# Kernel optimization log

Hardware: AMD Instinct MI355X
Metric: run time of the kernel (lower is better)

Reference implementation:

```python
import jax, jax.numpy as jnp
import numpy as np

N = 50000      # nodes
E = 800000     # edges (avg degree 16)
IN = 128       # in_dim = num_heads * out_dim
H = 8          # num_heads
D = 16         # out_dim per head
R = 9          # num_rels = num_bases


def setup_inputs() -> dict:
    key = jax.random.key(0)
    ks = jax.random.split(key, 13)
    sw = 1.0 / np.sqrt(IN)
    sc = 1.0 / np.sqrt(R)
    return {
        "h": jax.random.normal(ks[0], (N, IN), jnp.float32),
        "Qw": jax.random.normal(ks[1], (R, IN, IN), jnp.float32) * sw,
        "Qc": jax.random.normal(ks[2], (R, R), jnp.float32) * sc,
        "Qb": jax.random.normal(ks[3], (IN,), jnp.float32) * 0.02,
        "Kw": jax.random.normal(ks[4], (R, IN, IN), jnp.float32) * sw,
        "Kc": jax.random.normal(ks[5], (R, R), jnp.float32) * sc,
        "Kb": jax.random.normal(ks[6], (IN,), jnp.float32) * 0.02,
        "Vw": jax.random.normal(ks[7], (R, IN, IN), jnp.float32) * sw,
        "Vc": jax.random.normal(ks[8], (R, R), jnp.float32) * sc,
        "Vb": jax.random.normal(ks[9], (IN,), jnp.float32) * 0.02,
        "src": jax.random.randint(ks[10], (E,), 0, N, jnp.int32),
        "dst": jax.random.randint(ks[11], (E,), 0, N, jnp.int32),
        "etype": jax.random.randint(ks[12], (E,), 0, R, jnp.int32),
    }


def _rel_graph_conv(x, w_basis, comb, bias, src, dst, etype):
    # basis decomposition: W_r = sum_b comb[r,b] * basis[b]  -> [R, IN, IN]
    W = jnp.einsum("rb,bio->rio", comb, w_basis)
    # project node features under every relation once: [R, N, IN]
    xW = jnp.einsum("ni,rio->rno", x, W)
    # per-edge message m_e = W_{etype_e} x_{src_e}
    msg = xW[etype, src]                                   # [E, IN]
    agg = jax.ops.segment_sum(msg, dst, num_segments=N)    # sum over incoming edges
    return jax.nn.relu(agg + bias)                         # dropout = eval mode (identity)


def reference(h, Qw, Qc, Qb, Kw, Kc, Kb, Vw, Vc, Vb, src, dst, etype):
    Q = _rel_graph_conv(h, Qw, Qc, Qb, src, dst, etype).reshape(N, H, D)
    K = _rel_graph_conv(h, Kw, Kc, Kb, src, dst, etype).reshape(N, H, D)
    V = _rel_graph_conv(h, Vw, Vc, Vb, src, dst, etype).reshape(N, H, D)
    # edge attention score: (K_src . Q_dst) per head, scaled + clamped exp
    score = jnp.sum(K[src] * Q[dst], axis=-1, keepdims=True) / np.sqrt(D)  # [E, H, 1]
    score = jnp.exp(jnp.clip(score, -10.0, 10.0))
    # weighted-V aggregation and normalizer via segment sums over dst
    wV = jax.ops.segment_sum(V[src] * score, dst, num_segments=N)  # [N, H, D]
    z = jax.ops.segment_sum(score, dst, num_segments=N)            # [N, H, 1]
    return wV / (z + 1e-6)
```

## Files before the change

kernel.cpp:

```cpp
#include <hip/hip_runtime.h>

#define NN 50000
#define NE 800000
#define IND 128
#define NH 8
#define DH 16
#define NR 9
#define KTOT 1152
#define NOUT 384
#define OB_N 24
#define NBLK 196

typedef __attribute__((ext_vector_type(8))) short bf16x8;
typedef __attribute__((ext_vector_type(4))) float f32x4;

__device__ __forceinline__ ushort f2bf(float x) {
  unsigned u = __float_as_uint(x);
  u += 0x7FFF + ((u >> 16) & 1);
  return (ushort)(u >> 16);
}
__device__ __forceinline__ float bf2f(ushort h) {
  return __uint_as_float(((unsigned)h) << 16);
}

__global__ __launch_bounds__(256) void make_w(const float* __restrict__ Qw, const float* __restrict__ Qc,
                                              const float* __restrict__ Kw, const float* __restrict__ Kc,
                                              const float* __restrict__ Vw, const float* __restrict__ Vc,
                                              ushort* __restrict__ Wh, ushort* __restrict__ Wl) {
  int t = blockIdx.x * 256 + threadIdx.x;
  int k = t / NOUT;
  int og = t % NOUT;
  int r = k >> 7, i = k & 127;
  int m = og >> 7, oc = og & 127;
  const float* basis = m == 0 ? Qw : m == 1 ? Kw : Vw;
  const float* comb  = m == 0 ? Qc : m == 1 ? Kc : Vc;
  float w = 0.f;
#pragma unroll
  for (int b = 0; b < NR; ++b)
    w += comb[r * NR + b] * basis[(long)b * IND * IND + i * IND + oc];
  ushort hi = f2bf(w);
  ushort lo = f2bf(w - bf2f(hi));
  long idx = ((long)(k >> 5) * OB_N + (og >> 4)) * 512
           + (((k >> 3) & 3) * 16 + (og & 15)) * 8 + (k & 7);
  Wh[idx] = hi;
  Wl[idx] = lo;
}

__global__ __launch_bounds__(256) void hist_dst(const int* __restrict__ dst,
                                                int* __restrict__ deg) {
  int e = blockIdx.x * 256 + threadIdx.x;
  if (e < NE) atomicAdd(&deg[dst[e]], 1);
}

__global__ __launch_bounds__(256) void scan_p1(const int* __restrict__ deg,
                                               int* __restrict__ bsum) {
  __shared__ int sb[256];
  int t = threadIdx.x;
  int idx = blockIdx.x * 256 + t;
  int v = (idx < NN) ? deg[idx] : 0;
  sb[t] = v;
  __syncthreads();
  for (int off = 128; off > 0; off >>= 1) {
    if (t < off) sb[t] += sb[t + off];
    __syncthreads();
  }
  if (t == 0) bsum[blockIdx.x] = sb[0];
}

__global__ __launch_bounds__(256) void scan_p2(const int* __restrict__ bsum,
                                               int* __restrict__ boff,
                                               int* __restrict__ rowptr) {
  __shared__ int sb[256];
  int t = threadIdx.x;
  int v = (t < NBLK) ? bsum[t] : 0;
  sb[t] = v;
  __syncthreads();
  for (int off = 1; off < 256; off <<= 1) {
    int add = (t >= off) ? sb[t - off] : 0;
    __syncthreads();
    sb[t] += add;
    __syncthreads();
  }
  if (t < NBLK) boff[t] = sb[t] - v;
  if (t == 0) rowptr[NN] = NE;
}

__global__ __launch_bounds__(256) void scan_p3(const int* __restrict__ deg,
                                               const int* __restrict__ boff,
                                               int* __restrict__ rowptr,
                                               int* __restrict__ cursor) {
  __shared__ int sb[256];
  int t = threadIdx.x;
  int idx = blockIdx.x * 256 + t;
  int v = (idx < NN) ? deg[idx] : 0;
  sb[t] = v;
  __syncthreads();
  for (int off = 1; off < 256; off <<= 1) {
    int add = (t >= off) ? sb[t - off] : 0;
    __syncthreads();
    sb[t] += add;
    __syncthreads();
  }
  if (idx < NN) {
    int excl = sb[t] - v + boff[blockIdx.x];
    rowptr[idx] = excl;
    cursor[idx] = excl;
  }
}

__global__ __launch_bounds__(256) void bucket_edges(const int* __restrict__ src,
                                                    const int* __restrict__ dst,
                                                    const int* __restrict__ et,
                                                    int* __restrict__ cursor,
                                                    int* __restrict__ epk) {
  int e = blockIdx.x * 256 + threadIdx.x;
  if (e >= NE) return;
  int d = dst[e];
  int pos = atomicAdd(&cursor[d], 1);
  epk[pos] = src[e] | (et[e] << 20);
}

__global__ __launch_bounds__(256) void conv_agg(const float* __restrict__ x,
                                                const int* __restrict__ rowptr,
                                                const int* __restrict__ epk,
                                                ushort* __restrict__ Ah,
                                                ushort* __restrict__ Al,
                                                int rlo, int rhi) {
  int wid = (blockIdx.x * 256 + threadIdx.x) >> 6;
  int lane = threadIdx.x & 63;
  if (wid >= NN) return;
  float ax[NR], ay[NR];
#pragma unroll
  for (int rr = 0; rr < NR; ++rr) { ax[rr] = 0.f; ay[rr] = 0.f; }
  int r0 = rowptr[wid], r1 = rowptr[wid + 1];
  for (int base = r0; base < r1; base += 64) {
    int pe = (base + lane < r1) ? epk[base + lane] : 0;
    int cnt = min(64, r1 - base);
    for (int j = 0; j < cnt; ++j) {
      int p = __shfl(pe, j);
      int s = p & 0xFFFFF;
      int r = p >> 20;
      float2 xv = *(const float2*)(x + (long)s * IND + lane * 2);
#pragma unroll
      for (int rr = 0; rr < NR; ++rr)
        if (r == rr) { ax[rr] += xv.x; ay[rr] += xv.y; }
    }
  }
#pragma unroll
  for (int rr = 0; rr < NR; ++rr)
    if (rr >= rlo && rr < rhi) {
      ushort h0 = f2bf(ax[rr]);
      ushort l0 = f2bf(ax[rr] - bf2f(h0));
      ushort h1 = f2bf(ay[rr]);
      ushort l1 = f2bf(ay[rr] - bf2f(h1));
      long o = ((long)(rr - rlo) * NN + wid) * IND + lane * 2;
      *(unsigned*)(Ah + o) = (unsigned)h0 | ((unsigned)h1 << 16);
      *(unsigned*)(Al + o) = (unsigned)l0 | ((unsigned)l1 << 16);
    }
}

__global__ __launch_bounds__(512) void gemm_mfma(const ushort* __restrict__ Ah,
                                                 const ushort* __restrict__ Al,
                                                 const ushort* __restrict__ Wh,
                                                 const ushort* __restrict__ Wl,
                                                 const float* __restrict__ Qb,
                                                 const float* __restrict__ Kb,
                                                 const float* __restrict__ Vb,
                                                 float* __restrict__ F,
                                                 int nrel, int rlo, int first, int last) {
  const int tid = threadIdx.x;
  const int lane = tid & 63;
  const int wid = tid >> 6;
  const int wr = wid >> 2;
  const int wc = wid & 3;
  const int n0 = blockIdx.x * 128 + wr * 64;
  const int l15 = lane & 15;
  const int kg = lane >> 4;
  const int kgofs = kg * 8;

  long rowOff[4];
#pragma unroll
  for (int mi = 0; mi < 4; ++mi)
    rowOff[mi] = (long)min(n0 + mi * 16 + l15, NN - 1) * IND;

  const int nsteps = nrel * 4;

  f32x4 acc[4][6];
#pragma unroll
  for (int mi = 0; mi < 4; ++mi)
#pragma unroll
    for (int ni = 0; ni < 6; ++ni) acc[mi][ni] = (f32x4){0.f, 0.f, 0.f, 0.f};

  bf16x8 a0[8], a1[8], w[12];

  auto LOADA = [&](bf16x8* A, int s) {
    const long ab = ((long)(s >> 2) * NN) * IND + ((s & 3) * 32 + kgofs);
#pragma unroll
    for (int mi = 0; mi < 4; ++mi) {
      A[mi]     = *(const bf16x8*)(Ah + ab + rowOff[mi]);
      A[4 + mi] = *(const bf16x8*)(Al + ab + rowOff[mi]);
    }
  };
  auto LOADW = [&](bf16x8* W, int s) {
    const long wb = (((long)(rlo * 4 + s) * OB_N + wc * 6) * 64 + lane) * 8;
#pragma unroll
    for (int ni = 0; ni < 6; ++ni) {
      W[ni]     = *(const bf16x8*)(Wh + wb + ni * 512);
      W[6 + ni] = *(const bf16x8*)(Wl + wb + ni * 512);
    }
  };
  auto DOMFMA = [&](bf16x8* A, bf16x8* W) {
#pragma unroll
    for (int ni = 0; ni < 6; ++ni)
#pragma unroll
      for (int mi = 0; mi < 4; ++mi) {
        acc[mi][ni] = __builtin_amdgcn_mfma_f32_16x16x32_bf16(A[mi],     W[6 + ni], acc[mi][ni], 0, 0, 0);
        acc[mi][ni] = __builtin_amdgcn_mfma_f32_16x16x32_bf16(A[4 + mi], W[ni],     acc[mi][ni], 0, 0, 0);
        acc[mi][ni] = __builtin_amdgcn_mfma_f32_16x16x32_bf16(A[mi],     W[ni],     acc[mi][ni], 0, 0, 0);
      }
  };

  LOADA(a0, 0);
  LOADW(w, 0);
  for (int s = 0; s < nsteps; s += 2) {
    LOADA(a1, s + 1);
    DOMFMA(a0, w);
    LOADW(w, s + 1);
    if (s + 2 < nsteps) LOADA(a0, s + 2);
    DOMFMA(a1, w);
    if (s + 2 < nsteps) LOADW(w, s + 2);
  }

#pragma unroll
  for (int mi = 0; mi < 4; ++mi) {
#pragma unroll
    for (int ni = 0; ni < 6; ++ni) {
      int og = wc * 96 + ni * 16 + l15;
      int m = og >> 7, oc = og & 127;
      float b = (m == 0 ? Qb : m == 1 ? Kb : Vb)[oc];
      float* Fm = F + (long)m * NN * IND;
#pragma unroll
      for (int reg = 0; reg < 4; ++reg) {
        int n = n0 + mi * 16 + kg * 4 + reg;
        if (n < NN) {
          long fo = (long)n * IND + oc;
          float v = acc[mi][ni][reg];
          if (!first) v += Fm[fo];
          if (last) { v += b; v = v > 0.f ? v : 0.f; }
          Fm[fo] = v;
        }
      }
    }
  }
}

__global__ __launch_bounds__(256) void node_attn(const float* __restrict__ Q,
                                                 const float* __restrict__ K,
                                                 const float* __restrict__ V,
                                                 const int* __restrict__ rowptr,
                                                 const int* __restrict__ epk,
                                                 float* __restrict__ out) {
  int wid = (blockIdx.x * 256 + threadIdx.x) >> 6;
  int lane = threadIdx.x & 63;
  if (wid >= NN) return;
  float2 q = *(const float2*)(Q + (long)wid * IND + lane * 2);
  float accx = 0.f, accy = 0.f, zacc = 0.f;
  int r0 = rowptr[wid], r1 = rowptr[wid + 1];
  for (int base = r0; base < r1; base += 64) {
    int pe = (base + lane < r1) ? epk[base + lane] : 0;
    int cnt = min(64, r1 - base);
    for (int j = 0; j < cnt; ++j) {
      int s = __shfl(pe, j) & 0xFFFFF;
      float2 k = *(const float2*)(K + (long)s * IND + lane * 2);
      float2 v = *(const float2*)(V + (long)s * IND + lane * 2);
      float p = q.x * k.x + q.y * k.y;
      p += __shfl_xor(p, 1);
      p += __shfl_xor(p, 2);
      p += __shfl_xor(p, 4);
      float score = __expf(fminf(fmaxf(p * 0.25f, -10.f), 10.f));
      accx += score * v.x;
      accy += score * v.y;
      zacc += score;
    }
  }
  float inv = 1.f / (zacc + 1e-6f);
  *(float2*)(out + (long)wid * IND + lane * 2) = make_float2(accx * inv, accy * inv);
}

extern "C" void kernel_launch(void* const* d_in, const int* in_sizes, int n_in,
                              void* d_out, int out_size, void* d_ws, size_t ws_size,
                              hipStream_t stream) {
  const float* h  = (const float*)d_in[0];
  const float* Qw = (const float*)d_in[1];
  const float* Qc = (const float*)d_in[2];
  const float* Qb = (const float*)d_in[3];
  const float* Kw = (const float*)d_in[4];
  const float* Kc = (const float*)d_in[5];
  const float* Kb = (const float*)d_in[6];
  const float* Vw = (const float*)d_in[7];
  const float* Vc = (const float*)d_in[8];
  const float* Vb = (const float*)d_in[9];
  const int* src = (const int*)d_in[10];
  const int* dst = (const int*)d_in[11];
  const int* et  = (const int*)d_in[12];
  float* out = (float*)d_out;

  char* p = (char*)d_ws;
  ushort* Wh = (ushort*)p;  p += (long)KTOT * NOUT * 2;
  ushort* Wl = (ushort*)p;  p += (long)KTOT * NOUT * 2;
  float* F   = (float*)p;   p += 3L * NN * IND * 4;
  int* deg    = (int*)p;
  int* rowptr = deg + NN;
  int* cursor = rowptr + NN + 1;
  int* bsum   = cursor + NN;
  int* boff   = bsum + NBLK;
  int* epk    = boff + NBLK;
  long intbytes = (((long)(3 * NN + 1 + 2 * NBLK + NE)) * 4 + 15) & ~15L;
  p += intbytes;
  ushort* Ah = (ushort*)p;
  long fixed = (long)(p - (char*)d_ws);
  long per_rel = 2L * NN * IND * 2;
  int C = (int)(((long)ws_size - fixed) / per_rel);
  if (C > NR) C = NR;
  if (C < 1) C = 1;
  ushort* Al = Ah + (long)C * NN * IND;

  hipMemsetAsync(deg, 0, (size_t)NN * 4, stream);

  make_w<<<(KTOT * NOUT) / 256, 256, 0, stream>>>(Qw, Qc, Kw, Kc, Vw, Vc, Wh, Wl);

  const int eb = (NE + 255) / 256;
  hist_dst<<<eb, 256, 0, stream>>>(dst, deg);
  scan_p1<<<NBLK, 256, 0, stream>>>(deg, bsum);
  scan_p2<<<1, 256, 0, stream>>>(bsum, boff, rowptr);
  scan_p3<<<NBLK, 256, 0, stream>>>(deg, boff, rowptr, cursor);
  bucket_edges<<<eb, 256, 0, stream>>>(src, dst, et, cursor, epk);

  const int nwb = (NN * 64 + 255) / 256;
  const int gb  = (NN + 127) / 128;

  int first = 1;
  for (int rlo = 0; rlo < NR; rlo += C) {
    int rhi = rlo + C;
    if (rhi > NR) rhi = NR;
    conv_agg<<<nwb, 256, 0, stream>>>(h, rowptr, epk, Ah, Al, rlo, rhi);
    gemm_mfma<<<gb, 512, 0, stream>>>(Ah, Al, Wh, Wl, Qb, Kb, Vb, F,
                                      rhi - rlo, rlo, first, (rhi == NR) ? 1 : 0);
    first = 0;
  }

  node_attn<<<nwb, 256, 0, stream>>>(F, F + (long)NN * IND, F + 2L * NN * IND,
                                     rowptr, epk, out);
}
```

Baseline: 764.6 us.

## Fuse relation-wise neighbor aggregation into the MFMA GEMM via relation-sorted CSR

Adds a second CSR keyed by (relation, destination) and a fused kernel where each 64-node block gathers source features per relation into shared memory with LDS atomics. It then splits them to bf16 hi/lo and runs the MFMA GEMM directly, so the per-relation aggregates no longer pass through global memory. This removes the large Ah/Al intermediate buffers, the chunked multi-launch loop, and the read-modify-write of F across chunks. In exchange it adds a second histogram/scan/bucket pass over 450k bins, uses LDS atomics, and gives each block 9 serialized sync phases with smaller 64-row tiles.

Result: slower. 1.311 ms (+71.5%).

```diff
diff --git a/kernel.cpp b/kernel.cpp
--- a/kernel.cpp
+++ b/kernel.cpp
@@ -10,6 +10,8 @@
 #define NOUT 384
 #define OB_N 24
 #define NBLK 196
+#define NBINS2 450000
+#define NBLK2 1758
 
 typedef __attribute__((ext_vector_type(8))) short bf16x8;
 typedef __attribute__((ext_vector_type(4))) float f32x4;
@@ -120,122 +122,180 @@
   epk[pos] = src[e] | (et[e] << 20);
 }
 
-__global__ __launch_bounds__(256) void conv_agg(const float* __restrict__ x,
-                                                const int* __restrict__ rowptr,
-                                                const int* __restrict__ epk,
-                                                ushort* __restrict__ Ah,
-                                                ushort* __restrict__ Al,
-                                                int rlo, int rhi) {
-  int wid = (blockIdx.x * 256 + threadIdx.x) >> 6;
-  int lane = threadIdx.x & 63;
-  if (wid >= NN) return;
-  float ax[NR], ay[NR];
-#pragma unroll
-  for (int rr = 0; rr < NR; ++rr) { ax[rr] = 0.f; ay[rr] = 0.f; }
-  int r0 = rowptr[wid], r1 = rowptr[wid + 1];
-  for (int base = r0; base < r1; base += 64) {
-    int pe = (base + lane < r1) ? epk[base + lane] : 0;
-    int cnt = min(64, r1 - base);
-    for (int j = 0; j < cnt; ++j) {
-      int p = __shfl(pe, j);
-      int s = p & 0xFFFFF;
-      int r = p >> 20;
-      float2 xv = *(const float2*)(x + (long)s * IND + lane * 2);
-#pragma unroll
-      for (int rr = 0; rr < NR; ++rr)
-        if (r == rr) { ax[rr] += xv.x; ay[rr] += xv.y; }
+__global__ __launch_bounds__(256) void r_hist(const int* __restrict__ dst,
+                                              const int* __restrict__ et,
+                                              int* __restrict__ deg2) {
+  int e = blockIdx.x * 256 + threadIdx.x;
+  if (e < NE) atomicAdd(&deg2[et[e] * NN + dst[e]], 1);
+}
+
+__global__ __launch_bounds__(256) void r_p1(const int* __restrict__ deg2,
+                                            int* __restrict__ bsum2) {
+  __shared__ int sb[256];
+  int t = threadIdx.x;
+  int idx = blockIdx.x * 256 + t;
+  int v = (idx < NBINS2) ? deg2[idx] : 0;
+  sb[t] = v;
+  __syncthreads();
+  for (int off = 128; off > 0; off >>= 1) {
+    if (t < off) sb[t] += sb[t + off];
+    __syncthreads();
+  }
+  if (t == 0) bsum2[blockIdx.x] = sb[0];
+}
+
+__global__ __launch_bounds__(256) void r_p2(const int* __restrict__ bsum2,
+                                            int* __restrict__ boff2,
+                                            int* __restrict__ rowptr2) {
+  __shared__ int sb[256];
+  __shared__ int carry;
+  int t = threadIdx.x;
+  if (t == 0) carry = 0;
+  __syncthreads();
+  for (int c = 0; c < 7; ++c) {
+    int idx = c * 256 + t;
+    int v = (idx < NBLK2) ? bsum2[idx] : 0;
+    sb[t] = v;
+    __syncthreads();
+    for (int off = 1; off < 256; off <<= 1) {
+      int add = (t >= off) ? sb[t - off] : 0;
+      __syncthreads();
+      sb[t] += add;
+      __syncthreads();
     }
-  }
-#pragma unroll
-  for (int rr = 0; rr < NR; ++rr)
-    if (rr >= rlo && rr < rhi) {
-      ushort h0 = f2bf(ax[rr]);
-      ushort l0 = f2bf(ax[rr] - bf2f(h0));
-      ushort h1 = f2bf(ay[rr]);
-      ushort l1 = f2bf(ay[rr] - bf2f(h1));
-      long o = ((long)(rr - rlo) * NN + wid) * IND + lane * 2;
-      *(unsigned*)(Ah + o) = (unsigned)h0 | ((unsigned)h1 << 16);
-      *(unsigned*)(Al + o) = (unsigned)l0 | ((unsigned)l1 << 16);
-    }
-}
-
-__global__ __launch_bounds__(512) void gemm_mfma(const ushort* __restrict__ Ah,
-                                                 const ushort* __restrict__ Al,
-                                                 const ushort* __restrict__ Wh,
-                                                 const ushort* __restrict__ Wl,
-                                                 const float* __restrict__ Qb,
-                                                 const float* __restrict__ Kb,
-                                                 const float* __restrict__ Vb,
-                                                 float* __restrict__ F,
-                                                 int nrel, int rlo, int first, int last) {
+    if (idx < NBLK2) boff2[idx] = carry + sb[t] - v;
+    __syncthreads();
+    if (t == 0) carry += sb[255];
+    __syncthreads();
+  }
+  if (t == 0) rowptr2[NBINS2] = NE;
+}
+
+__global__ __launch_bounds__(256) void r_p3(const int* __restrict__ deg2,
+                                            const int* __restrict__ boff2,
+                                            int* __restrict__ rowptr2,
+                                            int* __restrict__ cursor2) {
+  __shared__ int sb[256];
+  int t = threadIdx.x;
+  int idx = blockIdx.x * 256 + t;
+  int v = (idx < NBINS2) ? deg2[idx] : 0;
+  sb[t] = v;
+  __syncthreads();
+  for (int off = 1; off < 256; off <<= 1) {
+    int add = (t >= off) ? sb[t - off] : 0;
+    __syncthreads();
+    sb[t] += add;
+    __syncthreads();
+  }
+  if (idx < NBINS2) {
+    int excl = sb[t] - v + boff2[blockIdx.x];
+    rowptr2[idx] = excl;
+    cursor2[idx] = excl;
+  }
+}
+
+__global__ __launch_bounds__(256) void r_bucket(const int* __restrict__ src,
+                                                const int* __restrict__ dst,
+                                                const int* __restrict__ et,
+                                                int* __restrict__ cursor2,
+                                                int* __restrict__ epk2) {
+  int e = blockIdx.x * 256 + threadIdx.x;
+  if (e >= NE) return;
+  int d = dst[e];
+  int pos = atomicAdd(&cursor2[et[e] * NN + d], 1);
+  epk2[pos] = src[e] | ((d & 63) << 20);
+}
+
+__global__ __launch_bounds__(256) void fused_gemm(const float* __restrict__ x,
+                                                  const int* __restrict__ rowptr2,
+                                                  const int* __restrict__ epk2,
+                                                  const ushort* __restrict__ Wh,
+                                                  const ushort* __restrict__ Wl,
+                                                  const float* __restrict__ Qb,
+                                                  const float* __restrict__ Kb,
+                                                  const float* __restrict__ Vb,
+                                                  float* __restrict__ F) {
+  __shared__ float As[64][132];
   const int tid = threadIdx.x;
   const int lane = tid & 63;
   const int wid = tid >> 6;
-  const int wr = wid >> 2;
-  const int wc = wid & 3;
-  const int n0 = blockIdx.x * 128 + wr * 64;
+  const int n0 = blockIdx.x * 64;
   const int l15 = lane & 15;
   const int kg = lane >> 4;
-  const int kgofs = kg * 8;
-
-  long rowOff[4];
+  const int nhi = min(n0 + 64, NN);
+  float* Af = &As[0][0];
+
+  f32x4 acc[4][6];
 #pragma unroll
   for (int mi = 0; mi < 4; ++mi)
-    rowOff[mi] = (long)min(n0 + mi * 16 + l15, NN - 1) * IND;
-
-  const int nsteps = nrel * 4;
-
-  f32x4 acc[4][6];
-#pragma unroll
-  for (int mi = 0; mi < 4; ++mi)
 #pragma unroll
     for (int ni = 0; ni < 6; ++ni) acc[mi][ni] = (f32x4){0.f, 0.f, 0.f, 0.f};
 
-  bf16x8 a0[8], a1[8], w[12];
-
-  auto LOADA = [&](bf16x8* A, int s) {
-    const long ab = ((long)(s >> 2) * NN) * IND + ((s & 3) * 32 + kgofs);
-#pragma unroll
-    for (int mi = 0; mi < 4; ++mi) {
-      A[mi]     = *(const bf16x8*)(Ah + ab + rowOff[mi]);
-      A[4 + mi] = *(const bf16x8*)(Al + ab + rowOff[mi]);
+  for (int r = 0; r < NR; ++r) {
+    __syncthreads();
+#pragma unroll
+    for (int k = 0; k < 33; ++k) Af[tid + k * 256] = 0.f;
+    __syncthreads();
+
+    const int lo = rowptr2[r * NN + n0];
+    const int hi = rowptr2[r * NN + nhi];
+    for (int e0 = lo; e0 < hi; e0 += 16) {
+      int e = e0 + wid * 4;
+      int p0 = (e     < hi) ? epk2[e]     : -1;
+      int p1 = (e + 1 < hi) ? epk2[e + 1] : -1;
+      int p2 = (e + 2 < hi) ? epk2[e + 2] : -1;
+      int p3 = (e + 3 < hi) ? epk2[e + 3] : -1;
+      float2 x0, x1, x2, x3;
+      if (p0 >= 0) x0 = *(const float2*)(x + (long)(p0 & 0xFFFFF) * IND + lane * 2);
+      if (p1 >= 0) x1 = *(const float2*)(x + (long)(p1 & 0xFFFFF) * IND + lane * 2);
+      if (p2 >= 0) x2 = *(const float2*)(x + (long)(p2 & 0xFFFFF) * IND + lane * 2);
+      if (p3 >= 0) x3 = *(const float2*)(x + (long)(p3 & 0xFFFFF) * IND + lane * 2);
+      if (p0 >= 0) { float* a = &As[p0 >> 20][lane * 2]; atomicAdd(a, x0.x); atomicAdd(a + 1, x0.y); }
+      if (p1 >= 0) { float* a = &As[p1 >> 20][lane * 2]; atomicAdd(a, x1.x); atomicAdd(a + 1, x1.y); }
+      if (p2 >= 0) { float* a = &As[p2 >> 20][lane * 2]; atomicAdd(a, x2.x); atomicAdd(a + 1, x2.y); }
+      if (p3 >= 0) { float* a = &As[p3 >> 20][lane * 2]; atomicAdd(a, x3.x); atomicAdd(a + 1, x3.y); }
     }
-  };
-  auto LOADW = [&](bf16x8* W, int s) {
-    const long wb = (((long)(rlo * 4 + s) * OB_N + wc * 6) * 64 + lane) * 8;
+    __syncthreads();
+
+#pragma unroll
+    for (int ks = 0; ks < 4; ++ks) {
+      bf16x8 w[12];
+      const long wb = (((long)(r * 4 + ks) * OB_N + wid * 6) * 64 + lane) * 8;
+#pragma unroll
+      for (int ni = 0; ni < 6; ++ni) {
+        w[ni]     = *(const bf16x8*)(Wh + wb + ni * 512);
+        w[6 + ni] = *(const bf16x8*)(Wl + wb + ni * 512);
+      }
+      bf16x8 ah[4], al[4];
+#pragma unroll
+      for (int mi = 0; mi < 4; ++mi) {
+        const float* pa = &As[mi * 16 + l15][ks * 32 + kg * 8];
+        float a[8];
+        *(float4*)&a[0] = *(const float4*)pa;
+        *(float4*)&a[4] = *(const float4*)(pa + 4);
+#pragma unroll
+        for (int j = 0; j < 8; ++j) {
+          ushort hb = f2bf(a[j]);
+          ah[mi][j] = (short)hb;
+          al[mi][j] = (short)f2bf(a[j] - bf2f(hb));
+        }
+      }
+#pragma unroll
+      for (int ni = 0; ni < 6; ++ni)
+#pragma unroll
+        for (int mi = 0; mi < 4; ++mi) {
+          acc[mi][ni] = __builtin_amdgcn_mfma_f32_16x16x32_bf16(ah[mi], w[6 + ni], acc[mi][ni], 0, 0, 0);
+          acc[mi][ni] = __builtin_amdgcn_mfma_f32_16x16x32_bf16(al[mi], w[ni],     acc[mi][ni], 0, 0, 0);
+          acc[mi][ni] = __builtin_amdgcn_mfma_f32_16x16x32_bf16(ah[mi], w[ni],     acc[mi][ni], 0, 0, 0);
+        }
+    }
+  }
+
+#pragma unroll
+  for (int mi = 0; mi < 4; ++mi) {
 #pragma unroll
     for (int ni = 0; ni < 6; ++ni) {
-      W[ni]     = *(const bf16x8*)(Wh + wb + ni * 512);
-      W[6 + ni] = *(const bf16x8*)(Wl + wb + ni * 512);
-    }
-  };
-  auto DOMFMA = [&](bf16x8* A, bf16x8* W) {
-#pragma unroll
-    for (int ni = 0; ni < 6; ++ni)
-#pragma unroll
-      for (int mi = 0; mi < 4; ++mi) {
-        acc[mi][ni] = __builtin_amdgcn_mfma_f32_16x16x32_bf16(A[mi],     W[6 + ni], acc[mi][ni], 0, 0, 0);
-        acc[mi][ni] = __builtin_amdgcn_mfma_f32_16x16x32_bf16(A[4 + mi], W[ni],     acc[mi][ni], 0, 0, 0);
-        acc[mi][ni] = __builtin_amdgcn_mfma_f32_16x16x32_bf16(A[mi],     W[ni],     acc[mi][ni], 0, 0, 0);
-      }
-  };
-
-  LOADA(a0, 0);
-  LOADW(w, 0);
-  for (int s = 0; s < nsteps; s += 2) {
-    LOADA(a1, s + 1);
-    DOMFMA(a0, w);
-    LOADW(w, s + 1);
-    if (s + 2 < nsteps) LOADA(a0, s + 2);
-    DOMFMA(a1, w);
-    if (s + 2 < nsteps) LOADW(w, s + 2);
-  }
-
-#pragma unroll
-  for (int mi = 0; mi < 4; ++mi) {
-#pragma unroll
-    for (int ni = 0; ni < 6; ++ni) {
-      int og = wc * 96 + ni * 16 + l15;
+      int og = wid * 96 + ni * 16 + l15;
       int m = og >> 7, oc = og & 127;
       float b = (m == 0 ? Qb : m == 1 ? Kb : Vb)[oc];
       float* Fm = F + (long)m * NN * IND;
@@ -243,11 +303,8 @@
       for (int reg = 0; reg < 4; ++reg) {
         int n = n0 + mi * 16 + kg * 4 + reg;
         if (n < NN) {
-          long fo = (long)n * IND + oc;
-          float v = acc[mi][ni][reg];
-          if (!first) v += Fm[fo];
-          if (last) { v += b; v = v > 0.f ? v : 0.f; }
-          Fm[fo] = v;
+          float v = acc[mi][ni][reg] + b;
+          Fm[(long)n * IND + oc] = v > 0.f ? v : 0.f;
         }
       }
     }
@@ -309,46 +366,40 @@
   ushort* Wh = (ushort*)p;  p += (long)KTOT * NOUT * 2;
   ushort* Wl = (ushort*)p;  p += (long)KTOT * NOUT * 2;
   float* F   = (float*)p;   p += 3L * NN * IND * 4;
-  int* deg    = (int*)p;
-  int* rowptr = deg + NN;
-  int* cursor = rowptr + NN + 1;
-  int* bsum   = cursor + NN;
-  int* boff   = bsum + NBLK;
-  int* epk    = boff + NBLK;
-  long intbytes = (((long)(3 * NN + 1 + 2 * NBLK + NE)) * 4 + 15) & ~15L;
-  p += intbytes;
-  ushort* Ah = (ushort*)p;
-  long fixed = (long)(p - (char*)d_ws);
-  long per_rel = 2L * NN * IND * 2;
-  int C = (int)(((long)ws_size - fixed) / per_rel);
-  if (C > NR) C = NR;
-  if (C < 1) C = 1;
-  ushort* Al = Ah + (long)C * NN * IND;
+  int* deg     = (int*)p;
+  int* rowptr  = deg + NN;
+  int* cursor  = rowptr + NN + 1;
+  int* bsum    = cursor + NN;
+  int* boff    = bsum + NBLK;
+  int* epk     = boff + NBLK;
+  int* deg2    = epk + NE;
+  int* rowptr2 = deg2 + NBINS2;
+  int* cursor2 = rowptr2 + NBINS2 + 1;
+  int* bsum2   = cursor2 + NBINS2;
+  int* boff2   = bsum2 + NBLK2;
+  int* epk2    = boff2 + NBLK2;
 
   hipMemsetAsync(deg, 0, (size_t)NN * 4, stream);
+  hipMemsetAsync(deg2, 0, (size_t)NBINS2 * 4, stream);
 
   make_w<<<(KTOT * NOUT) / 256, 256, 0, stream>>>(Qw, Qc, Kw, Kc, Vw, Vc, Wh, Wl);
 
   const int eb = (NE + 255) / 256;
   hist_dst<<<eb, 256, 0, stream>>>(dst, deg);
+  r_hist<<<eb, 256, 0, stream>>>(dst, et, deg2);
   scan_p1<<<NBLK, 256, 0, stream>>>(deg, bsum);
   scan_p2<<<1, 256, 0, stream>>>(bsum, boff, rowptr);
   scan_p3<<<NBLK, 256, 0, stream>>>(deg, boff, rowptr, cursor);
   bucket_edges<<<eb, 256, 0, stream>>>(src, dst, et, cursor, epk);
+  r_p1<<<NBLK2, 256, 0, stream>>>(deg2, bsum2);
+  r_p2<<<1, 256, 0, stream>>>(bsum2, boff2, rowptr2);
+  r_p3<<<NBLK2, 256, 0, stream>>>(deg2, boff2, rowptr2, cursor2);
+  r_bucket<<<eb, 256, 0, stream>>>(src, dst, et, cursor2, epk2);
+
+  fused_gemm<<<(NN + 63) / 64, 256, 0, stream>>>(h, rowptr2, epk2, Wh, Wl,
+                                                 Qb, Kb, Vb, F);
 
   const int nwb = (NN * 64 + 255) / 256;
-  const int gb  = (NN + 127) / 128;
-
-  int first = 1;
-  for (int rlo = 0; rlo < NR; rlo += C) {
-    int rhi = rlo + C;
-    if (rhi > NR) rhi = NR;
-    conv_agg<<<nwb, 256, 0, stream>>>(h, rowptr, epk, Ah, Al, rlo, rhi);
-    gemm_mfma<<<gb, 512, 0, stream>>>(Ah, Al, Wh, Wl, Qb, Kb, Vb, F,
-                                      rhi - rlo, rlo, first, (rhi == NR) ? 1 : 0);
-    first = 0;
-  }
-
   node_attn<<<nwb, 256, 0, stream>>>(F, F + (long)NN * IND, F + 2L * NN * IND,
                                      rowptr, epk, out);
 }
```
